# Optimization experiments

Hardware: AMD Instinct MI355X
Metric: run time of the kernel (lower is better)

## Reference

```python
import jax, jax.numpy as jnp
import numpy as np

N = 100000   # nodes of type 'A'
D = 128      # embedding_dim and input feature dim
E = 1600000  # edges per metapath (avg degree 16)
R = 2        # metapaths with head type 'A'; beta has R+1 channels (self)


def setup_inputs() -> dict:
    key = jax.random.key(0)
    ks = jax.random.split(key, 8)
    s = 1.0 / np.sqrt(D)
    return {
        "x": jax.random.normal(ks[0], (N, D), jnp.float32),
        "edge_index_r1": jax.random.randint(ks[1], (2, E), 0, N),
        "edge_index_r2": jax.random.randint(ks[2], (2, E), 0, N),
        "W_lin": jax.random.normal(ks[3], (D, D), jnp.float32) * s,
        "b_lin": jnp.zeros((D,), jnp.float32),
        "W_conv": jax.random.normal(ks[4], (R + 1, D), jnp.float32) * s,  # kernel-size-1 Conv1d == linear
        "b_conv": jnp.zeros((R + 1,), jnp.float32),
        "attn_l_w": jax.random.normal(ks[5], (R, D), jnp.float32) * s,
        "attn_l_b": jnp.zeros((R,), jnp.float32),
        "attn_r_w": jax.random.normal(ks[6], (R, D), jnp.float32) * s,
        "attn_r_b": jnp.zeros((R,), jnp.float32),
        "alpha_weights": jnp.ones((R,), jnp.float32),
    }


def _segment_softmax(logits, seg, n):
    mx = jax.ops.segment_max(logits, seg, num_segments=n)
    mx = jnp.where(jnp.isfinite(mx), mx, 0.0)  # empty segments
    ex = jnp.exp(logits - mx[seg])
    denom = jax.ops.segment_sum(ex, seg, num_segments=n)
    return ex / (denom[seg] + 1e-16)


def reference(x, edge_index_r1, edge_index_r2, W_lin, b_lin, W_conv, b_conv,
              attn_l_w, attn_l_b, attn_r_w, attn_r_b, alpha_weights):
    n = x.shape[0]
    h = x @ W_lin.T + b_lin                              # get_h_dict: Linear
    beta = jax.nn.softmax(x @ W_conv.T + b_conv, axis=1)  # [N, R+1] relation weights
    al = x @ jnp.zeros((0,)) if False else h @ attn_l_w.T + attn_l_b  # [N, R]
    ar = h @ attn_r_w.T + attn_r_b                        # [N, R]
    rels = []
    for m, ei in enumerate((edge_index_r1, edge_index_r2)):
        dst, src = ei[0], ei[1]  # flow='target_to_source': aggregate into edge_index[0]
        logit = alpha_weights[m] * (al[src, m] + ar[dst, m])  # [E]
        att = _segment_softmax(logit, dst, n)
        rels.append(jax.ops.segment_sum(h[src] * att[:, None], dst, num_segments=n))
    rel = jnp.stack(rels + [h], axis=1)                   # [N, R+1, D], last slot = self
    out = jnp.einsum("nrd,nr->nd", rel, beta)            # matmul(perm, beta).squeeze
    return jax.nn.relu(out)                               # activation='relu'
```

## Files before the change

kernel.cpp:

```cpp
#include <hip/hip_runtime.h>

#define DIM 128
#define NSL 128
#define WMAX 25000

typedef __attribute__((ext_vector_type(8))) short bf16x8;
typedef __attribute__((ext_vector_type(4))) float f32x4;

__device__ __forceinline__ unsigned bfbits(float f) {
    unsigned u = __float_as_uint(f);
    return (u + 0x7FFFu + ((u >> 16) & 1u)) >> 16;
}
__device__ __forceinline__ float bflo(unsigned u) { return __uint_as_float(u << 16); }
__device__ __forceinline__ float bfhi(unsigned u) { return __uint_as_float(u & 0xFFFF0000u); }

__global__ __launch_bounds__(256) void k_gemm_h(
    const float* __restrict__ x, const float* __restrict__ W,
    const float* __restrict__ b, const float* __restrict__ Wc,
    const float* __restrict__ bcv, const float* __restrict__ alw,
    const float* __restrict__ alb, const float* __restrict__ alpha,
    unsigned short* __restrict__ h2u, float* __restrict__ exal0,
    float* __restrict__ exal1, float* __restrict__ betab, int n)
{
    __shared__ short wlds[128 * 136];
    __shared__ short xlds[64 * 136];
    const int tid  = threadIdx.x;
    const int row0 = blockIdx.x * 64;

    {
        const int j = tid >> 1, half = tid & 1;
        const float4* W4 = (const float4*)W;
#pragma unroll
        for (int i = 0; i < 8; ++i) {
            float4 fa = W4[j * 32 + half * 16 + i * 2];
            float4 fb = W4[j * 32 + half * 16 + i * 2 + 1];
            uint4 p;
            p.x = bfbits(fa.x) | (bfbits(fa.y) << 16);
            p.y = bfbits(fa.z) | (bfbits(fa.w) << 16);
            p.z = bfbits(fb.x) | (bfbits(fb.y) << 16);
            p.w = bfbits(fb.z) | (bfbits(fb.w) << 16);
            *(uint4*)&wlds[j * 136 + half * 64 + i * 8] = p;
        }
    }
    {
        const int r = tid >> 2, q = tid & 3;
        const int row = min(row0 + r, n - 1);
        const float4* x4 = (const float4*)x;
#pragma unroll
        for (int i = 0; i < 4; ++i) {
            float4 fa = x4[(size_t)row * 32 + q * 8 + i * 2];
            float4 fb = x4[(size_t)row * 32 + q * 8 + i * 2 + 1];
            uint4 p;
            p.x = bfbits(fa.x) | (bfbits(fa.y) << 16);
            p.y = bfbits(fa.z) | (bfbits(fa.w) << 16);
            p.z = bfbits(fb.x) | (bfbits(fb.y) << 16);
            p.w = bfbits(fb.z) | (bfbits(fb.w) << 16);
            *(uint4*)&xlds[r * 136 + q * 32 + i * 8] = p;
        }
    }
    __syncthreads();

    const int wv = tid >> 6, lane = tid & 63;
    const int lr = lane & 15, lg = lane >> 4;

    f32x4 acc[8];
#pragma unroll
    for (int c = 0; c < 8; ++c) acc[c] = (f32x4){0.f, 0.f, 0.f, 0.f};

#pragma unroll
    for (int ks = 0; ks < 4; ++ks) {
        bf16x8 a = *(const bf16x8*)&xlds[(wv * 16 + lr) * 136 + ks * 32 + lg * 8];
#pragma unroll
        for (int c = 0; c < 8; ++c) {
            bf16x8 bb = *(const bf16x8*)&wlds[(c * 16 + lr) * 136 + ks * 32 + lg * 8];
            acc[c] = __builtin_amdgcn_mfma_f32_16x16x32_bf16(a, bb, acc[c], 0, 0, 0);
        }
    }

    const int rl0 = wv * 16 + lg * 4;
    float as0[4] = {0.f,0.f,0.f,0.f}, as1[4] = {0.f,0.f,0.f,0.f};
#pragma unroll
    for (int c = 0; c < 8; ++c) {
        const int col = c * 16 + lr;
        const float bc = b[col];
        const float w0 = alw[col], w1 = alw[128 + col];
#pragma unroll
        for (int r = 0; r < 4; ++r) {
            const float hv = acc[c][r] + bc;
            const int row = row0 + rl0 + r;
            if (row < n)
                h2u[(size_t)row * DIM + col] = (unsigned short)bfbits(hv);
            as0[r] = fmaf(hv, w0, as0[r]);
            as1[r] = fmaf(hv, w1, as1[r]);
        }
    }
    float xs0[4] = {0.f,0.f,0.f,0.f}, xs1[4] = {0.f,0.f,0.f,0.f},
          xs2[4] = {0.f,0.f,0.f,0.f};
#pragma unroll
    for (int i = 0; i < 8; ++i) {
        const int col = lr + i * 16;
        const float wc0 = Wc[col], wc1 = Wc[128 + col], wc2 = Wc[256 + col];
#pragma unroll
        for (int r = 0; r < 4; ++r) {
            const float xv = bflo((unsigned)(unsigned short)xlds[(rl0 + r) * 136 + col]);
            xs0[r] = fmaf(xv, wc0, xs0[r]);
            xs1[r] = fmaf(xv, wc1, xs1[r]);
            xs2[r] = fmaf(xv, wc2, xs2[r]);
        }
    }
#pragma unroll
    for (int o = 1; o <= 8; o <<= 1) {
#pragma unroll
        for (int r = 0; r < 4; ++r) {
            as0[r] += __shfl_xor(as0[r], o);
            as1[r] += __shfl_xor(as1[r], o);
            xs0[r] += __shfl_xor(xs0[r], o);
            xs1[r] += __shfl_xor(xs1[r], o);
            xs2[r] += __shfl_xor(xs2[r], o);
        }
    }
    if (lr == 0) {
        const float a0 = alpha[0], a1 = alpha[1];
        const float ab0 = alb[0], ab1 = alb[1];
        const float b0 = bcv[0], b1 = bcv[1], b2 = bcv[2];
#pragma unroll
        for (int r = 0; r < 4; ++r) {
            const int row = row0 + rl0 + r;
            if (row < n) {
                exal0[row] = __expf(a0 * (as0[r] + ab0));
                exal1[row] = __expf(a1 * (as1[r] + ab1));
                float c0 = xs0[r] + b0, c1 = xs1[r] + b1, c2 = xs2[r] + b2;
                float mx = fmaxf(c0, fmaxf(c1, c2));
                float e0 = __expf(c0 - mx), e1 = __expf(c1 - mx),
                      e2 = __expf(c2 - mx);
                float s = e0 + e1 + e2;
                betab[row * 3 + 0] = e0 / s;
                betab[row * 3 + 1] = e1 / s;
                betab[row * 3 + 2] = e2 / s;
            }
        }
    }
}

__global__ __launch_bounds__(1024) void k_hist(
    const int* __restrict__ ei1, const int* __restrict__ ei2,
    unsigned* __restrict__ pb, int n, int e)
{
    __shared__ unsigned lds[WMAX];
    const int blk = blockIdx.x;
    const int s   = blk % NSL;
    const int m   = blk / NSL;
    const int* ei = m ? ei2 : ei1;
    const int W   = (n + 3) >> 2;

    for (int i = threadIdx.x; i < W; i += 1024) lds[i] = 0;
    __syncthreads();

    const int sl = (e + NSL - 1) / NSL;
    const int j0 = s * sl, j1 = min(j0 + sl, e);
    for (int j = j0 + threadIdx.x; j < j1; j += 1024) {
        int d = ei[j];
        atomicAdd(&lds[d >> 2], 1u << ((d & 3) * 8));
    }
    __syncthreads();

    unsigned* dst = pb + (size_t)blk * WMAX;
    for (int i = threadIdx.x; i < W; i += 1024) dst[i] = lds[i];
}

__global__ __launch_bounds__(256) void k_combine(
    unsigned* __restrict__ pb, int* __restrict__ cnt, int n)
{
    const int W = (n + 3) >> 2;
    int t = blockIdx.x * 256 + threadIdx.x;
    if (t >= 2 * W) return;
    const int m = t / W, w = t % W;

    unsigned run = 0;
    unsigned* base = pb + ((size_t)m * NSL) * WMAX + w;
    for (int s = 0; s < NSL; ++s) {
        unsigned v = base[(size_t)s * WMAX];
        base[(size_t)s * WMAX] = run;
        run += v;
    }
    int bin = 4 * w;
    if (bin + 3 < n) {
        int4 c = make_int4(run & 0xFF, (run >> 8) & 0xFF,
                           (run >> 16) & 0xFF, (run >> 24) & 0xFF);
        *(int4*)&cnt[m * n + bin] = c;
    } else {
        for (int j = 0; j < 4 && bin + j < n; ++j)
            cnt[m * n + bin + j] = (run >> (8 * j)) & 0xFF;
    }
}

__global__ __launch_bounds__(256) void k_scan1(
    const int* __restrict__ cnt, int* __restrict__ excl,
    int* __restrict__ bsum, int n2)
{
    __shared__ int sh[256];
    int t = threadIdx.x;
    int base = blockIdx.x * 1024 + t * 4;
    int v0 = (base + 0 < n2) ? cnt[base + 0] : 0;
    int v1 = (base + 1 < n2) ? cnt[base + 1] : 0;
    int v2 = (base + 2 < n2) ? cnt[base + 2] : 0;
    int v3 = (base + 3 < n2) ? cnt[base + 3] : 0;
    int s1 = v0 + v1, s2 = s1 + v2, s3 = s2 + v3;
    sh[t] = s3;
    __syncthreads();
    for (int off = 1; off < 256; off <<= 1) {
        int a = (t >= off) ? sh[t - off] : 0;
        __syncthreads();
        sh[t] += a;
        __syncthreads();
    }
    int eb = sh[t] - s3;
    if (t == 255) bsum[blockIdx.x] = sh[255];
    if (base + 0 < n2) excl[base + 0] = eb;
    if (base + 1 < n2) excl[base + 1] = eb + v0;
    if (base + 2 < n2) excl[base + 2] = eb + s1;
    if (base + 3 < n2) excl[base + 3] = eb + s2;
}

__global__ __launch_bounds__(256) void k_scan2(int* __restrict__ bsum, int nb)
{
    __shared__ int sh[256];
    int t = threadIdx.x;
    int v = (t < nb) ? bsum[t] : 0;
    sh[t] = v;
    __syncthreads();
    for (int off = 1; off < 256; off <<= 1) {
        int a = (t >= off) ? sh[t - off] : 0;
        __syncthreads();
        sh[t] += a;
        __syncthreads();
    }
    if (t < nb) bsum[t] = sh[t] - v;
}

__global__ __launch_bounds__(256) void k_scan3(
    int* __restrict__ rp, const int* __restrict__ bsum, int n2, int etot)
{
    int i = blockIdx.x * 256 + threadIdx.x;
    if (i < n2) rp[i] += bsum[i >> 10];
    if (i == 0) rp[n2] = etot;
}

__global__ __launch_bounds__(1024) void k_fill(
    const int* __restrict__ ei1, const int* __restrict__ ei2,
    const unsigned* __restrict__ pb, const int* __restrict__ rp,
    int* __restrict__ srcs, int n, int e)
{
    __shared__ unsigned lds[WMAX];
    const int blk = blockIdx.x;
    const int s   = blk % NSL;
    const int m   = blk / NSL;
    const int* ei = m ? ei2 : ei1;
    const int W   = (n + 3) >> 2;

    for (int i = threadIdx.x; i < W; i += 1024) lds[i] = 0;
    __syncthreads();

    const unsigned* sb = pb + (size_t)blk * WMAX;
    const int sl = (e + NSL - 1) / NSL;
    const int j0 = s * sl, j1 = min(j0 + sl, e);
    for (int j = j0 + threadIdx.x; j < j1; j += 1024) {
        int d  = ei[j];
        int sv = ei[e + j];
        int sh = (d & 3) * 8;
        unsigned old = atomicAdd(&lds[d >> 2], 1u << sh);
        int rank = (old >> sh) & 0xFF;
        int bse  = (sb[d >> 2] >> sh) & 0xFF;
        srcs[rp[m * n + d] + bse + rank] = sv;
    }
}

__global__ __launch_bounds__(256) void k_gather(
    const unsigned* __restrict__ h2,
    const float* __restrict__ exal0, const float* __restrict__ exal1,
    const float* __restrict__ betab,
    const int* __restrict__ rp, const int* __restrict__ srcs,
    float* __restrict__ out, int n)
{
    int wid  = blockIdx.x * 4 + (threadIdx.x >> 6);
    if (wid >= n) return;
    int lane = threadIdx.x & 63;

    float b0 = betab[wid * 3 + 0];
    float b1 = betab[wid * 3 + 1];
    float b2 = betab[wid * 3 + 2];

    float2 acc;
    {
        unsigned hu = h2[(size_t)wid * 64 + lane];
        acc.x = b2 * bflo(hu);
        acc.y = b2 * bfhi(hu);
    }

#pragma unroll
    for (int m = 0; m < 2; ++m) {
        const int s0 = rp[m * n + wid];
        const int s1 = rp[m * n + wid + 1];
        const float* exal = m ? exal1 : exal0;
        const float bm = m ? b1 : b0;

        float sum = 0.0f;
        float2 a = {0.0f, 0.0f};

        for (int base = s0; base < s1; base += 64) {
            const int cnt = min(64, s1 - base);

            int   src = 0;
            float ex  = 0.0f;
            if (lane < cnt) {
                src = srcs[base + lane];
                ex  = exal[src];
            }
            {
                float t = ex;
#pragma unroll
                for (int o = 32; o > 0; o >>= 1) t += __shfl_xor(t, o);
                sum += t;
            }

            const unsigned exu = __float_as_uint(ex);
            int j = 0;
            for (; j + 8 <= cnt; j += 8) {
                unsigned u[8];
                float    w[8];
#pragma unroll
                for (int q = 0; q < 8; ++q) {
                    int s = __builtin_amdgcn_readlane(src, j + q);
                    w[q]  = __uint_as_float(__builtin_amdgcn_readlane(exu, j + q));
                    u[q]  = h2[(size_t)s * 64 + lane];
                }
#pragma unroll
                for (int q = 0; q < 8; ++q) {
                    a.x = fmaf(w[q], bflo(u[q]), a.x);
                    a.y = fmaf(w[q], bfhi(u[q]), a.y);
                }
            }
            for (; j + 2 <= cnt; j += 2) {
                int   sA = __builtin_amdgcn_readlane(src, j + 0);
                int   sB = __builtin_amdgcn_readlane(src, j + 1);
                float wA = __uint_as_float(__builtin_amdgcn_readlane(exu, j + 0));
                float wB = __uint_as_float(__builtin_amdgcn_readlane(exu, j + 1));
                unsigned uA = h2[(size_t)sA * 64 + lane];
                unsigned uB = h2[(size_t)sB * 64 + lane];
                a.x = fmaf(wA, bflo(uA), a.x); a.y = fmaf(wA, bfhi(uA), a.y);
                a.x = fmaf(wB, bflo(uB), a.x); a.y = fmaf(wB, bfhi(uB), a.y);
            }
            if (j < cnt) {
                int   sA = __builtin_amdgcn_readlane(src, j);
                float wA = __uint_as_float(__builtin_amdgcn_readlane(exu, j));
                unsigned uA = h2[(size_t)sA * 64 + lane];
                a.x = fmaf(wA, bflo(uA), a.x);
                a.y = fmaf(wA, bfhi(uA), a.y);
            }
        }

        float sc = bm / (sum + 1e-16f);
        acc.x = fmaf(sc, a.x, acc.x);
        acc.y = fmaf(sc, a.y, acc.y);
    }

    float2 o;
    o.x = fmaxf(acc.x, 0.0f);
    o.y = fmaxf(acc.y, 0.0f);
    *(float2*)(out + (size_t)wid * DIM + lane * 2) = o;
}

extern "C" void kernel_launch(void* const* d_in, const int* in_sizes, int n_in,
                              void* d_out, int out_size, void* d_ws, size_t ws_size,
                              hipStream_t stream)
{
    const float* x     = (const float*)d_in[0];
    const int*   ei1   = (const int*)d_in[1];
    const int*   ei2   = (const int*)d_in[2];
    const float* W_lin = (const float*)d_in[3];
    const float* b_lin = (const float*)d_in[4];
    const float* W_cv  = (const float*)d_in[5];
    const float* b_cv  = (const float*)d_in[6];
    const float* alw   = (const float*)d_in[7];
    const float* alb   = (const float*)d_in[8];
    const float* alpha = (const float*)d_in[11];

    const int N  = in_sizes[0] / DIM;
    const int E  = in_sizes[1] / 2;
    const int N2 = 2 * N;
    const int W  = (N + 3) >> 2;

    float* out = (float*)d_out;

    unsigned* h2    = (unsigned*)d_ws;
    float*    exal0 = (float*)(h2 + (size_t)N * 64);
    float*    exal1 = exal0 + N;
    float*    betab = exal1 + N;
    int*      rp    = (int*)(betab + (size_t)3 * N);
    int*      cnt   = rp + (N2 + 2);
    int*      bsum  = cnt + N2;
    unsigned* pb    = (unsigned*)(bsum + 256);
    int*      srcs  = (int*)(pb + (size_t)2 * NSL * WMAX);

    const int nb = (N2 + 1023) / 1024;

    k_gemm_h<<<(N + 63) / 64, 256, 0, stream>>>(x, W_lin, b_lin, W_cv, b_cv,
                                                alw, alb, alpha,
                                                (unsigned short*)h2,
                                                exal0, exal1, betab, N);

    k_hist<<<2 * NSL, 1024, 0, stream>>>(ei1, ei2, pb, N, E);

    k_combine<<<(2 * W + 255) / 256, 256, 0, stream>>>(pb, cnt, N);

    k_scan1<<<nb, 256, 0, stream>>>(cnt, rp, bsum, N2);
    k_scan2<<<1, 256, 0, stream>>>(bsum, nb);
    k_scan3<<<(N2 + 255) / 256, 256, 0, stream>>>(rp, bsum, N2, 2 * E);

    k_fill<<<2 * NSL, 1024, 0, stream>>>(ei1, ei2, pb, rp, srcs, N, E);

    k_gather<<<(N + 3) / 4, 256, 0, stream>>>(h2, exal0, exal1, betab,
                                              rp, srcs, out, N);
}
```

Measured before the change: 272.6 us.

## Split each wavefront into four 16-lane groups gathering edges with 16-byte loads

The gather kernel now splits each 64-lane wavefront into four 16-lane groups. Each group handles a different edge and loads a full 256-byte bf16 row with uint4 loads, instead of all lanes reading one 4-byte word per edge. Partial sums are reduced across the groups with xor shuffles at the end, and packed f32x2 FMAs are used. This is meant to raise memory-level parallelism and cut per-edge instruction overhead, at the cost of shuffles (ds_bpermute) replacing readlane and a final cross-group reduction.

```diff
diff --git a/kernel.cpp b/kernel.cpp
--- a/kernel.cpp
+++ b/kernel.cpp
@@ -6,6 +6,7 @@
 
 typedef __attribute__((ext_vector_type(8))) short bf16x8;
 typedef __attribute__((ext_vector_type(4))) float f32x4;
+typedef __attribute__((ext_vector_type(2))) float f32x2;
 
 __device__ __forceinline__ unsigned bfbits(float f) {
     unsigned u = __float_as_uint(f);
@@ -284,18 +285,17 @@
 {
     int wid  = blockIdx.x * 4 + (threadIdx.x >> 6);
     if (wid >= n) return;
-    int lane = threadIdx.x & 63;
+    const int lane = threadIdx.x & 63;
+    const int g    = lane >> 4;
+    const int q    = lane & 15;
 
     float b0 = betab[wid * 3 + 0];
     float b1 = betab[wid * 3 + 1];
     float b2 = betab[wid * 3 + 2];
 
-    float2 acc;
-    {
-        unsigned hu = h2[(size_t)wid * 64 + lane];
-        acc.x = b2 * bflo(hu);
-        acc.y = b2 * bfhi(hu);
-    }
+    f32x2 acc[4];
+#pragma unroll
+    for (int c = 0; c < 4; ++c) acc[c] = (f32x2){0.f, 0.f};
 
 #pragma unroll
     for (int m = 0; m < 2; ++m) {
@@ -305,7 +305,9 @@
         const float bm = m ? b1 : b0;
 
         float sum = 0.0f;
-        float2 a = {0.0f, 0.0f};
+        f32x2 ap[4];
+#pragma unroll
+        for (int c = 0; c < 4; ++c) ap[c] = (f32x2){0.f, 0.f};
 
         for (int base = s0; base < s1; base += 64) {
             const int cnt = min(64, s1 - base);
@@ -323,51 +325,79 @@
                 sum += t;
             }
 
-            const unsigned exu = __float_as_uint(ex);
             int j = 0;
             for (; j + 8 <= cnt; j += 8) {
-                unsigned u[8];
-                float    w[8];
-#pragma unroll
-                for (int q = 0; q < 8; ++q) {
-                    int s = __builtin_amdgcn_readlane(src, j + q);
-                    w[q]  = __uint_as_float(__builtin_amdgcn_readlane(exu, j + q));
-                    u[q]  = h2[(size_t)s * 64 + lane];
+                int   sA = __shfl(src, j + g);
+                int   sB = __shfl(src, j + 4 + g);
+                float wA = __shfl(ex,  j + g);
+                float wB = __shfl(ex,  j + 4 + g);
+                const uint4 uA = *(const uint4*)(h2 + (size_t)sA * 64 + q * 4);
+                const uint4 uB = *(const uint4*)(h2 + (size_t)sB * 64 + q * 4);
+                f32x2 wa = {wA, wA}, wb = {wB, wB};
+                ap[0] = __builtin_elementwise_fma(wa, (f32x2){bflo(uA.x), bfhi(uA.x)}, ap[0]);
+                ap[1] = __builtin_elementwise_fma(wa, (f32x2){bflo(uA.y), bfhi(uA.y)}, ap[1]);
+                ap[2] = __builtin_elementwise_fma(wa, (f32x2){bflo(uA.z), bfhi(uA.z)}, ap[2]);
+                ap[3] = __builtin_elementwise_fma(wa, (f32x2){bflo(uA.w), bfhi(uA.w)}, ap[3]);
+                ap[0] = __builtin_elementwise_fma(wb, (f32x2){bflo(uB.x), bfhi(uB.x)}, ap[0]);
+                ap[1] = __builtin_elementwise_fma(wb, (f32x2){bflo(uB.y), bfhi(uB.y)}, ap[1]);
+                ap[2] = __builtin_elementwise_fma(wb, (f32x2){bflo(uB.z), bfhi(uB.z)}, ap[2]);
+                ap[3] = __builtin_elementwise_fma(wb, (f32x2){bflo(uB.w), bfhi(uB.w)}, ap[3]);
+            }
+            for (; j + 4 <= cnt; j += 4) {
+                int   sA = __shfl(src, j + g);
+                float wA = __shfl(ex,  j + g);
+                const uint4 uA = *(const uint4*)(h2 + (size_t)sA * 64 + q * 4);
+                f32x2 wa = {wA, wA};
+                ap[0] = __builtin_elementwise_fma(wa, (f32x2){bflo(uA.x), bfhi(uA.x)}, ap[0]);
+                ap[1] = __builtin_elementwise_fma(wa, (f32x2){bflo(uA.y), bfhi(uA.y)}, ap[1]);
+                ap[2] = __builtin_elementwise_fma(wa, (f32x2){bflo(uA.z), bfhi(uA.z)}, ap[2]);
+                ap[3] = __builtin_elementwise_fma(wa, (f32x2){bflo(uA.w), bfhi(uA.w)}, ap[3]);
+            }
+            {
+                const int rem = cnt - j;
+                int   sA = __shfl(src, j + (g < rem ? g : 0));
+                float wA = __shfl(ex,  j + (g < rem ? g : 0));
+                if (g < rem) {
+                    const uint4 uA = *(const uint4*)(h2 + (size_t)sA * 64 + q * 4);
+                    f32x2 wa = {wA, wA};
+                    ap[0] = __builtin_elementwise_fma(wa, (f32x2){bflo(uA.x), bfhi(uA.x)}, ap[0]);
+                    ap[1] = __builtin_elementwise_fma(wa, (f32x2){bflo(uA.y), bfhi(uA.y)}, ap[1]);
+                    ap[2] = __builtin_elementwise_fma(wa, (f32x2){bflo(uA.z), bfhi(uA.z)}, ap[2]);
+                    ap[3] = __builtin_elementwise_fma(wa, (f32x2){bflo(uA.w), bfhi(uA.w)}, ap[3]);
                 }
-#pragma unroll
-                for (int q = 0; q < 8; ++q) {
-                    a.x = fmaf(w[q], bflo(u[q]), a.x);
-                    a.y = fmaf(w[q], bfhi(u[q]), a.y);
-                }
-            }
-            for (; j + 2 <= cnt; j += 2) {
-                int   sA = __builtin_amdgcn_readlane(src, j + 0);
-                int   sB = __builtin_amdgcn_readlane(src, j + 1);
-                float wA = __uint_as_float(__builtin_amdgcn_readlane(exu, j + 0));
-                float wB = __uint_as_float(__builtin_amdgcn_readlane(exu, j + 1));
-                unsigned uA = h2[(size_t)sA * 64 + lane];
-                unsigned uB = h2[(size_t)sB * 64 + lane];
-                a.x = fmaf(wA, bflo(uA), a.x); a.y = fmaf(wA, bfhi(uA), a.y);
-                a.x = fmaf(wB, bflo(uB), a.x); a.y = fmaf(wB, bfhi(uB), a.y);
-            }
-            if (j < cnt) {
-                int   sA = __builtin_amdgcn_readlane(src, j);
-                float wA = __uint_as_float(__builtin_amdgcn_readlane(exu, j));
-                unsigned uA = h2[(size_t)sA * 64 + lane];
-                a.x = fmaf(wA, bflo(uA), a.x);
-                a.y = fmaf(wA, bfhi(uA), a.y);
-            }
-        }
-
-        float sc = bm / (sum + 1e-16f);
-        acc.x = fmaf(sc, a.x, acc.x);
-        acc.y = fmaf(sc, a.y, acc.y);
-    }
-
-    float2 o;
-    o.x = fmaxf(acc.x, 0.0f);
-    o.y = fmaxf(acc.y, 0.0f);
-    *(float2*)(out + (size_t)wid * DIM + lane * 2) = o;
+            }
+        }
+
+        const float sc = bm / (sum + 1e-16f);
+        f32x2 s2 = {sc, sc};
+#pragma unroll
+        for (int c = 0; c < 4; ++c)
+            acc[c] = __builtin_elementwise_fma(s2, ap[c], acc[c]);
+    }
+
+#pragma unroll
+    for (int o = 16; o <= 32; o <<= 1) {
+#pragma unroll
+        for (int c = 0; c < 4; ++c) {
+            acc[c].x += __shfl_xor(acc[c].x, o);
+            acc[c].y += __shfl_xor(acc[c].y, o);
+        }
+    }
+
+    if (g == 0) {
+        const uint4 su = *(const uint4*)(h2 + (size_t)wid * 64 + q * 4);
+        float4 o0, o1;
+        o0.x = fmaxf(fmaf(b2, bflo(su.x), acc[0].x), 0.0f);
+        o0.y = fmaxf(fmaf(b2, bfhi(su.x), acc[0].y), 0.0f);
+        o0.z = fmaxf(fmaf(b2, bflo(su.y), acc[1].x), 0.0f);
+        o0.w = fmaxf(fmaf(b2, bfhi(su.y), acc[1].y), 0.0f);
+        o1.x = fmaxf(fmaf(b2, bflo(su.z), acc[2].x), 0.0f);
+        o1.y = fmaxf(fmaf(b2, bfhi(su.z), acc[2].y), 0.0f);
+        o1.z = fmaxf(fmaf(b2, bflo(su.w), acc[3].x), 0.0f);
+        o1.w = fmaxf(fmaf(b2, bfhi(su.w), acc[3].y), 0.0f);
+        *(float4*)(out + (size_t)wid * DIM + q * 8)     = o0;
+        *(float4*)(out + (size_t)wid * DIM + q * 8 + 4) = o1;
+    }
 }
 
 extern "C" void kernel_launch(void* const* d_in, const int* in_sizes, int n_in,
```

Result: no change. 275.6 us (+1.1%).
